# Optimization experiments

Measured on AMD Instinct MI355X. Metric: run time of the kernel, lower is better.

Reference implementation:

```python
import jax, jax.numpy as jnp
import numpy as np


def setup_inputs() -> dict:
    key = jax.random.key(0)
    k1, k2 = jax.random.split(key)
    feature_map = jax.random.normal(k1, (1, 64, 64, 1024), dtype=jnp.float32)
    # (x, y, w, h) per ROI; +1 ensures w,h >= 1 and keeps crops inside the 64x64 map
    rois = jax.random.randint(k2, (1, 300, 4), 0, 31, dtype=jnp.int32) + 1
    return {"feature_map": feature_map, "rois": rois, "pool_size": 14}


def reference(feature_map, rois, pool_size):
    """RoiPoolingConv: per-ROI crop + legacy-TF bilinear resize to (P, P).

    tf.image.resize_images (TF1, align_corners=False, no half-pixel centers)
    samples src = dst * (in_size / out_size); the upper bilinear index is
    clamped to in_size - 1. Cropping then resizing equals sampling the full
    map at y + dst*h/P (resp. x + dst*w/P) with the clamp at y+h-1 / x+w-1.
    """
    fm = feature_map[0]  # [H, W, C] -- module hardcodes batch index 0 via rois[0]
    P = pool_size
    grid = jnp.arange(P, dtype=jnp.float32)

    def sample_one_roi(roi):
        x, y, w, h = roi[0], roi[1], roi[2], roi[3]  # int32 scalars
        fy = y.astype(jnp.float32) + grid * (h.astype(jnp.float32) / P)  # [P]
        fx = x.astype(jnp.float32) + grid * (w.astype(jnp.float32) / P)  # [P]
        y0 = jnp.floor(fy).astype(jnp.int32)
        x0 = jnp.floor(fx).astype(jnp.int32)
        y1 = jnp.minimum(y0 + 1, y + h - 1)
        x1 = jnp.minimum(x0 + 1, x + w - 1)
        wy = (fy - y0.astype(jnp.float32))[:, None, None]  # [P,1,1]
        wx = (fx - x0.astype(jnp.float32))[None, :, None]  # [1,P,1]
        tl = fm[y0][:, x0]  # [P, P, C]
        tr = fm[y0][:, x1]
        bl = fm[y1][:, x0]
        br = fm[y1][:, x1]
        top = tl + wx * (tr - tl)
        bot = bl + wx * (br - bl)
        return top + wy * (bot - top)  # [P, P, C]

    out = jax.vmap(sample_one_roi)(rois[0])  # [num_rois, P, P, C]
    return out[None]  # [1, num_rois, P, P, C]
```

## Files before the change

### kernel.cpp

```cpp
#include <hip/hip_runtime.h>


#define POOL 14
#define FMW 64
#define CH 1024
#define C4 (CH / 4)

typedef float f4 __attribute__((ext_vector_type(4)));

__global__ __launch_bounds__(256) void roi_pool_row_kernel(
    const float* __restrict__ fm,
    const int* __restrict__ rois,
    float* __restrict__ out)
{
    const int NW  = 300 * POOL;
    const int per = NW / 8;
    const int b   = blockIdx.x;
    const int sb  = (b % 8) * per + (b / 8);

    const int py  = sb % POOL;
    const int roi = sb / POOL;

    const int4 r = *reinterpret_cast<const int4*>(rois + roi * 4);
    const int x = r.x, y = r.y, w = r.z, h = r.w;

    const float fy = (float)y + (float)py * ((float)h * (1.0f / 14.0f));
    const int   y0 = (int)floorf(fy);
    const int   y1 = min(y0 + 1, y + h - 1);
    const float wy = fy - (float)y0;

    const int c = threadIdx.x;
    const f4* row0 = reinterpret_cast<const f4*>(fm) + (size_t)y0 * FMW * C4 + c;
    const f4* row1 = reinterpret_cast<const f4*>(fm) + (size_t)y1 * FMW * C4 + c;
    f4* op = reinterpret_cast<f4*>(out) + ((size_t)roi * POOL + py) * POOL * C4 + c;

    const float wscale = (float)w * (1.0f / 14.0f);

    #pragma unroll 2
    for (int px = 0; px < POOL; ++px) {
        const float fx = (float)x + (float)px * wscale;
        const int   x0 = (int)floorf(fx);
        const int   x1 = min(x0 + 1, x + w - 1);
        const float wx = fx - (float)x0;

        const f4 tl = row0[(size_t)x0 * C4];
        const f4 tr = row0[(size_t)x1 * C4];
        const f4 bl = row1[(size_t)x0 * C4];
        const f4 br = row1[(size_t)x1 * C4];

        const f4 top = tl + wx * (tr - tl);
        const f4 bot = bl + wx * (br - bl);
        const f4 o   = top + wy * (bot - top);

        __builtin_nontemporal_store(o, op + (size_t)px * C4);
    }
}

extern "C" void kernel_launch(void* const* d_in, const int* in_sizes, int n_in,
                              void* d_out, int out_size, void* d_ws, size_t ws_size,
                              hipStream_t stream) {
    const float* fm  = (const float*)d_in[0];
    const int* rois  = (const int*)d_in[1];
    float* out       = (float*)d_out;

    const int num_rois = in_sizes[1] / 4;
    const int blocks = num_rois * POOL;
    roi_pool_row_kernel<<<blocks, 256, 0, stream>>>(fm, rois, out);
}
```

Before: 64.34 us.

## Sort ROI rows by source feature-map row before pooling for cache locality

Adds a single-block counting-sort kernel that buckets all (roi, py) work items by their top source row y0 and writes a permutation to the workspace. The pooling kernel then processes items in that order, still using the XCD-aware block swizzle, so blocks that read the same feature-map rows are scheduled close together and can share L2. The cost is an extra kernel launch with atomics and a serial prefix sum, plus one more indirection per block. A fallback kernel keeps the old order when the workspace is too small or the item count is not divisible by eight.

```diff
diff --git a/kernel.cpp b/kernel.cpp
--- a/kernel.cpp
+++ b/kernel.cpp
@@ -8,15 +8,99 @@
 
 typedef float f4 __attribute__((ext_vector_type(4)));
 
+__global__ __launch_bounds__(1024) void sort_items_kernel(
+    const int* __restrict__ rois, int num_items, int* __restrict__ perm)
+{
+    __shared__ int base[64];
+    const int tid = threadIdx.x;
+
+    if (tid < 64) base[tid] = 0;
+    __syncthreads();
+
+    for (int i = tid; i < num_items; i += blockDim.x) {
+        const int roi = i / POOL, py = i % POOL;
+        const int y = rois[roi * 4 + 1], h = rois[roi * 4 + 3];
+        const float fy = (float)y + (float)py * ((float)h * (1.0f / 14.0f));
+        const int y0 = (int)floorf(fy);
+        atomicAdd(&base[y0 & 63], 1);
+    }
+    __syncthreads();
+
+    if (tid == 0) {
+        int s = 0;
+        for (int k = 0; k < 64; ++k) { int c = base[k]; base[k] = s; s += c; }
+    }
+    __syncthreads();
+
+    for (int i = tid; i < num_items; i += blockDim.x) {
+        const int roi = i / POOL, py = i % POOL;
+        const int y = rois[roi * 4 + 1], h = rois[roi * 4 + 3];
+        const float fy = (float)y + (float)py * ((float)h * (1.0f / 14.0f));
+        const int y0 = (int)floorf(fy);
+        const int pos = atomicAdd(&base[y0 & 63], 1);
+        perm[pos] = i;
+    }
+}
+
 __global__ __launch_bounds__(256) void roi_pool_row_kernel(
     const float* __restrict__ fm,
     const int* __restrict__ rois,
+    const int* __restrict__ perm,
+    int nw,
     float* __restrict__ out)
 {
-    const int NW  = 300 * POOL;
-    const int per = NW / 8;
+    const int per = nw >> 3;
     const int b   = blockIdx.x;
-    const int sb  = (b % 8) * per + (b / 8);
+    const int sb  = (b & 7) * per + (b >> 3);
+    const int item = perm[sb];
+
+    const int py  = item % POOL;
+    const int roi = item / POOL;
+
+    const int4 r = *reinterpret_cast<const int4*>(rois + roi * 4);
+    const int x = r.x, y = r.y, w = r.z, h = r.w;
+
+    const float fy = (float)y + (float)py * ((float)h * (1.0f / 14.0f));
+    const int   y0 = (int)floorf(fy);
+    const int   y1 = min(y0 + 1, y + h - 1);
+    const float wy = fy - (float)y0;
+
+    const int c = threadIdx.x;
+    const f4* row0 = reinterpret_cast<const f4*>(fm) + (size_t)y0 * FMW * C4 + c;
+    const f4* row1 = reinterpret_cast<const f4*>(fm) + (size_t)y1 * FMW * C4 + c;
+    f4* op = reinterpret_cast<f4*>(out) + ((size_t)roi * POOL + py) * POOL * C4 + c;
+
+    const float wscale = (float)w * (1.0f / 14.0f);
+
+    #pragma unroll 2
+    for (int px = 0; px < POOL; ++px) {
+        const float fx = (float)x + (float)px * wscale;
+        const int   x0 = (int)floorf(fx);
+        const int   x1 = min(x0 + 1, x + w - 1);
+        const float wx = fx - (float)x0;
+
+        const f4 tl = row0[(size_t)x0 * C4];
+        const f4 tr = row0[(size_t)x1 * C4];
+        const f4 bl = row1[(size_t)x0 * C4];
+        const f4 br = row1[(size_t)x1 * C4];
+
+        const f4 top = tl + wx * (tr - tl);
+        const f4 bot = bl + wx * (br - bl);
+        const f4 o   = top + wy * (bot - top);
+
+        __builtin_nontemporal_store(o, op + (size_t)px * C4);
+    }
+}
+
+__global__ __launch_bounds__(256) void roi_pool_row_kernel_noperm(
+    const float* __restrict__ fm,
+    const int* __restrict__ rois,
+    int nw,
+    float* __restrict__ out)
+{
+    const int per = nw >> 3;
+    const int b   = blockIdx.x;
+    const int sb  = (nw & 7) ? b : (b & 7) * per + (b >> 3);
 
     const int py  = sb % POOL;
     const int roi = sb / POOL;
@@ -64,6 +148,13 @@
     float* out       = (float*)d_out;
 
     const int num_rois = in_sizes[1] / 4;
-    const int blocks = num_rois * POOL;
-    roi_pool_row_kernel<<<blocks, 256, 0, stream>>>(fm, rois, out);
+    const int nw = num_rois * POOL;
+
+    if (ws_size >= (size_t)nw * sizeof(int) && (nw & 7) == 0) {
+        int* perm = (int*)d_ws;
+        sort_items_kernel<<<1, 1024, 0, stream>>>(rois, nw, perm);
+        roi_pool_row_kernel<<<nw, 256, 0, stream>>>(fm, rois, perm, nw, out);
+    } else {
+        roi_pool_row_kernel_noperm<<<nw, 256, 0, stream>>>(fm, rois, nw, out);
+    }
 }
```

Measured after the change: 60.18 us. -6.5%, faster.
